# Kernel optimization log

Hardware: AMD Instinct MI355X
Metric: run time of the kernel (lower is better)

The kernel has to match this reference:

```python
import jax, jax.numpy as jnp
import numpy as np

H, DH = 8, 40            # heads, dim_head -> inner_dim = 320
SCALE = DH ** -0.5
B, N, M = 16, 4096, 77   # batch, query tokens (64x64 latent), text tokens
QD, CD, ID = 320, 768, H * DH


def setup_inputs() -> dict:
    key = jax.random.key(0)
    ks = jax.random.split(key, 7)
    x = jax.random.normal(ks[0], (B, N, QD), dtype=jnp.float32)
    context = jax.random.normal(ks[1], (B, M, CD), dtype=jnp.float32)
    # Linear weights stored as (in, out); torch nn.Linear has no bias for q/k/v
    Wq = jax.random.normal(ks[2], (QD, ID), dtype=jnp.float32) * (QD ** -0.5)
    Wk = jax.random.normal(ks[3], (CD, ID), dtype=jnp.float32) * (CD ** -0.5)
    Wv = jax.random.normal(ks[4], (CD, ID), dtype=jnp.float32) * (CD ** -0.5)
    Wo = jax.random.normal(ks[5], (ID, QD), dtype=jnp.float32) * (ID ** -0.5)
    bo = jnp.zeros((QD,), dtype=jnp.float32)
    return {"x": x, "context": context, "Wq": Wq, "Wk": Wk, "Wv": Wv, "Wo": Wo, "bo": bo}


def reference(x, context, Wq, Wk, Wv, Wo, bo):
    b, n, _ = x.shape
    m = context.shape[1]
    q = (x @ Wq).reshape(b, n, H, DH)        # to_q
    k = (context @ Wk).reshape(b, m, H, DH)  # to_k
    v = (context @ Wv).reshape(b, m, H, DH)  # to_v
    # full QK^T * scale (rank-bias path inactive: rank={} / is_add_rank=False)
    scores = jnp.einsum('bihd,bjhd->bhij', q, k) * SCALE  # [B,H,N,M]
    attn = jax.nn.softmax(scores, axis=-1)
    out = jnp.einsum('bhij,bjhd->bihd', attn, v).reshape(b, n, ID)
    return out @ Wo + bo  # to_out Linear; Dropout(p=0.0) is identity
```

## Files before the change

### kernel.cpp

```cpp
#include <hip/hip_runtime.h>

typedef unsigned short u16;
using short8 = __attribute__((ext_vector_type(8))) short;
using f32x4  = __attribute__((ext_vector_type(4))) float;

#define SCALE 0.15811388300841897f

__device__ __forceinline__ u16 f2bf(float f) {
  unsigned int u = __float_as_uint(f);
  u += 0x7fffu + ((u >> 16) & 1u);
  return (u16)(u >> 16);
}


__global__ void prep_transpose(const float* __restrict__ Wq, const float* __restrict__ Wo,
                               const float* __restrict__ Wk, const float* __restrict__ Wv,
                               u16* __restrict__ wqt, u16* __restrict__ wot,
                               u16* __restrict__ wkt, u16* __restrict__ wvt) {
  __shared__ float ld[64][65];
  const int bid = blockIdx.x;
  const float* src; u16* dst; int K; float scale; int tk, tn;
  if (bid < 25)       { src = Wq; dst = wqt; K = 320; scale = SCALE; tk = bid / 5;         tn = bid % 5; }
  else if (bid < 50)  { src = Wo; dst = wot; K = 320; scale = 1.f;   tk = (bid - 25) / 5;  tn = (bid - 25) % 5; }
  else if (bid < 110) { src = Wk; dst = wkt; K = 768; scale = 1.f;   tk = (bid - 50) / 5;  tn = (bid - 50) % 5; }
  else                { src = Wv; dst = wvt; K = 768; scale = 1.f;   tk = (bid - 110) / 5; tn = (bid - 110) % 5; }
  const int c = threadIdx.x & 63, r0 = threadIdx.x >> 6;
  for (int rr = r0; rr < 64; rr += 4)
    ld[rr][c] = src[(size_t)(tk * 64 + rr) * 320 + tn * 64 + c];
  __syncthreads();
  for (int rr = r0; rr < 64; rr += 4)
    dst[(size_t)(tn * 64 + rr) * K + tk * 64 + c] = f2bf(ld[c][rr] * scale);
}

__global__ __launch_bounds__(512, 1)
void kv_mfma(const float* __restrict__ ctx,
             const u16* __restrict__ wkt, const u16* __restrict__ wvt,
             u16* __restrict__ kbf, u16* __restrict__ vt) {
  const int b = blockIdx.x;
  const int tid = threadIdx.x;
  const int w = tid >> 6, l = tid & 63, l16 = l & 15, lhi = l >> 4;
  __shared__ __align__(16) u16 sctx[80][776];

  for (int i = tid; i < 80 * 192; i += 512) {
    int row = i / 192, c4 = (i - row * 192) * 4;
    ushort4 u;
    if (row < 77) {
      float4 v = *reinterpret_cast<const float4*>(&ctx[(size_t)(b * 77 + row) * 768 + c4]);
      u.x = f2bf(v.x); u.y = f2bf(v.y); u.z = f2bf(v.z); u.w = f2bf(v.w);
    } else u = (ushort4){0, 0, 0, 0};
    *reinterpret_cast<ushort4*>(&sctx[row][c4]) = u;
  }
  for (int i = tid; i < 8 * 80 * 3; i += 512) {
    int hm = i / 3, q = i - hm * 3;
    int h = hm / 80, m = hm - h * 80;
    *reinterpret_cast<uint4*>(&kbf[(((size_t)b * 8 + h) * 80 + m) * 64 + 40 + q * 8]) = (uint4){0, 0, 0, 0};
  }
  for (int i = tid; i < 8 * 48 * 2; i += 512) {
    int hd = i / 2, q = i - hd * 2;
    int h = hd / 48, d = hd - h * 48;
    *reinterpret_cast<uint4*>(&vt[(((size_t)b * 8 + h) * 48 + d) * 96 + 80 + q * 8]) = (uint4){0, 0, 0, 0};
  }
  for (int i = tid; i < 8 * 8 * 10; i += 512) {
    int h = i / 80, rem = i - h * 80;
    int d = 40 + rem / 10, q = rem - (rem / 10) * 10;
    *reinterpret_cast<uint4*>(&vt[(((size_t)b * 8 + h) * 48 + d) * 96 + q * 8]) = (uint4){0, 0, 0, 0};
  }
  __syncthreads();

  f32x4 acc[5][5];
  #pragma unroll
  for (int rt = 0; rt < 5; ++rt)
    #pragma unroll
    for (int nt = 0; nt < 5; ++nt) acc[rt][nt] = (f32x4){0.f, 0.f, 0.f, 0.f};

  const u16* wbase = (w < 4) ? (wkt + (size_t)(w * 80) * 768)
                             : (wvt + (size_t)((w - 4) * 80) * 768);
  #pragma unroll 2
  for (int ks = 0; ks < 24; ++ks) {
    short8 af[5];
    #pragma unroll
    for (int rt = 0; rt < 5; ++rt)
      af[rt] = *reinterpret_cast<const short8*>(&sctx[rt * 16 + l16][ks * 32 + lhi * 8]);
    short8 bf[5];
    #pragma unroll
    for (int nt = 0; nt < 5; ++nt)
      bf[nt] = *reinterpret_cast<const short8*>(&wbase[(size_t)(nt * 16 + l16) * 768 + ks * 32 + lhi * 8]);
    #pragma unroll
    for (int rt = 0; rt < 5; ++rt)
      #pragma unroll
      for (int nt = 0; nt < 5; ++nt)
        acc[rt][nt] = __builtin_amdgcn_mfma_f32_16x16x32_bf16(af[rt], bf[nt], acc[rt][nt], 0, 0, 0);
  }

  if (w < 4) {
    #pragma unroll
    for (int rt = 0; rt < 5; ++rt)
      #pragma unroll
      for (int nt = 0; nt < 5; ++nt) {
        int c = w * 80 + nt * 16 + l16, h = c / 40, d = c - h * 40;
        #pragma unroll
        for (int r = 0; r < 4; ++r) {
          int m = rt * 16 + lhi * 4 + r;
          kbf[(((size_t)b * 8 + h) * 80 + m) * 64 + d] = f2bf(m < 77 ? acc[rt][nt][r] : 0.f);
        }
      }
  } else {
    #pragma unroll
    for (int rt = 0; rt < 5; ++rt)
      #pragma unroll
      for (int nt = 0; nt < 5; ++nt) {
        int c = (w - 4) * 80 + nt * 16 + l16, h = c / 40, d = c - h * 40;
        #pragma unroll
        for (int r = 0; r < 4; ++r) {
          int m = rt * 16 + lhi * 4 + r;
          vt[(((size_t)b * 8 + h) * 48 + d) * 96 + m] = f2bf(m < 77 ? acc[rt][nt][r] : 0.f);
        }
      }
  }
}

__global__ __launch_bounds__(256, 3)
void qproj(const float* __restrict__ x, const u16* __restrict__ wqt,
           u16* __restrict__ qg) {
  const int tid = threadIdx.x;
  const int w = tid >> 6, l = tid & 63, l16 = l & 15, lhi = l >> 4;
  const int r0 = blockIdx.x * 64;
  __shared__ __align__(16) u16 xs[64][328];

  const float4* xin = reinterpret_cast<const float4*>(x + (size_t)r0 * 320);
  for (int i = tid; i < 64 * 80; i += 256) {
    float4 v = xin[i];
    int row = i / 80, c4 = (i - row * 80) * 4;
    ushort4 u;
    u.x = f2bf(v.x); u.y = f2bf(v.y); u.z = f2bf(v.z); u.w = f2bf(v.w);
    *reinterpret_cast<ushort4*>(&xs[row][c4]) = u;
  }
  if (blockIdx.x == 1023 && tid < 64) qg[(size_t)65536 * 320 + tid] = 0;
  __syncthreads();

  f32x4 acc[4][5];
  #pragma unroll
  for (int rt = 0; rt < 4; ++rt)
    #pragma unroll
    for (int nt = 0; nt < 5; ++nt) acc[rt][nt] = (f32x4){0.f, 0.f, 0.f, 0.f};
  #pragma unroll 2
  for (int ks = 0; ks < 10; ++ks) {
    short8 af[4];
    #pragma unroll
    for (int rt = 0; rt < 4; ++rt)
      af[rt] = *reinterpret_cast<const short8*>(&xs[rt * 16 + l16][ks * 32 + lhi * 8]);
    #pragma unroll
    for (int nt = 0; nt < 5; ++nt) {
      short8 bf = *reinterpret_cast<const short8*>(&wqt[(size_t)(w * 80 + nt * 16 + l16) * 320 + ks * 32 + lhi * 8]);
      #pragma unroll
      for (int rt = 0; rt < 4; ++rt)
        acc[rt][nt] = __builtin_amdgcn_mfma_f32_16x16x32_bf16(af[rt], bf, acc[rt][nt], 0, 0, 0);
    }
  }
  #pragma unroll
  for (int rt = 0; rt < 4; ++rt)
    #pragma unroll
    for (int nt = 0; nt < 5; ++nt) {
      int col = w * 80 + nt * 16 + l16;
      #pragma unroll
      for (int r = 0; r < 4; ++r) {
        int row = rt * 16 + lhi * 4 + r;
        qg[(size_t)(r0 + row) * 320 + col] = f2bf(acc[rt][nt][r]);
      }
    }
}

__global__ __launch_bounds__(512, 8)
void attn_sm(u16* __restrict__ qg, const u16* __restrict__ kbf,
             const u16* __restrict__ vtp) {
  const int b  = blockIdx.y;
  const int q0 = blockIdx.x * 64;
  const int tid = threadIdx.x;
  const int w   = tid >> 6;
  const int l   = tid & 63;
  const int l16 = l & 15;
  const int lhi = l >> 4;
  const int wq  = w & 3;
  const int hg  = w >> 2;

  __shared__ __align__(16) u16 Pt[8][16][104];

  if (l < 32) {
    int r = l >> 1, q = l & 1;
    *reinterpret_cast<uint4*>(&Pt[w][r][80 + 8 * q]) = (uint4){0u, 0u, 0u, 0u};
  }

  const size_t rowbase = (size_t)(b * 4096 + q0 + wq * 16);

  for (int hi = 0; hi < 4; ++hi) {
    const int h = hg * 4 + hi;
    const u16* kh = kbf + ((size_t)(b * 8 + h)) * 80 * 64;
    const u16* vh = vtp + ((size_t)(b * 8 + h)) * 48 * 96;
    f32x4 sacc[5];
    #pragma unroll
    for (int mt = 0; mt < 5; ++mt) sacc[mt] = (f32x4){0.f, 0.f, 0.f, 0.f};
    #pragma unroll
    for (int ks = 0; ks < 2; ++ks) {
      short8 a = *reinterpret_cast<const short8*>(
          &qg[(rowbase + l16) * 320 + h * 40 + ks * 32 + lhi * 8]);
      #pragma unroll
      for (int mt = 0; mt < 5; ++mt) {
        short8 bb = *reinterpret_cast<const short8*>(&kh[(mt * 16 + l16) * 64 + ks * 32 + lhi * 8]);
        sacc[mt] = __builtin_amdgcn_mfma_f32_16x16x32_bf16(a, bb, sacc[mt], 0, 0, 0);
      }
    }
    #pragma unroll
    for (int r = 0; r < 4; ++r) {
      float sv[5];
      float mx = -1e30f;
      #pragma unroll
      for (int mt = 0; mt < 5; ++mt) {
        float s = sacc[mt][r];
        if (mt * 16 + l16 >= 77) s = -1e30f;
        sv[mt] = s;
        mx = fmaxf(mx, s);
      }
      mx = fmaxf(mx, __shfl_xor(mx, 1));
      mx = fmaxf(mx, __shfl_xor(mx, 2));
      mx = fmaxf(mx, __shfl_xor(mx, 4));
      mx = fmaxf(mx, __shfl_xor(mx, 8));
      float sum = 0.f;
      #pragma unroll
      for (int mt = 0; mt < 5; ++mt) { sv[mt] = __expf(sv[mt] - mx); sum += sv[mt]; }
      sum += __shfl_xor(sum, 1);
      sum += __shfl_xor(sum, 2);
      sum += __shfl_xor(sum, 4);
      sum += __shfl_xor(sum, 8);
      float rs = 1.f / sum;
      int row = lhi * 4 + r;
      #pragma unroll
      for (int mt = 0; mt < 5; ++mt)
        Pt[w][row][mt * 16 + l16] = f2bf(sv[mt] * rs);
    }
    asm volatile("s_waitcnt lgkmcnt(0)" ::: "memory");
    __builtin_amdgcn_sched_barrier(0);
    f32x4 oacc[3];
    #pragma unroll
    for (int nt = 0; nt < 3; ++nt) oacc[nt] = (f32x4){0.f, 0.f, 0.f, 0.f};
    #pragma unroll
    for (int ks = 0; ks < 3; ++ks) {
      short8 a = *reinterpret_cast<const short8*>(&Pt[w][l16][ks * 32 + lhi * 8]);
      #pragma unroll
      for (int nt = 0; nt < 3; ++nt) {
        short8 bb = *reinterpret_cast<const short8*>(&vh[(nt * 16 + l16) * 96 + ks * 32 + lhi * 8]);
        oacc[nt] = __builtin_amdgcn_mfma_f32_16x16x32_bf16(a, bb, oacc[nt], 0, 0, 0);
      }
    }
    asm volatile("s_waitcnt lgkmcnt(0)" ::: "memory");
    __builtin_amdgcn_sched_barrier(0);
    #pragma unroll
    for (int nt = 0; nt < 3; ++nt) {
      int d = nt * 16 + l16;
      if (d < 40) {
        #pragma unroll
        for (int r = 0; r < 4; ++r)
          qg[(rowbase + lhi * 4 + r) * 320 + h * 40 + d] = f2bf(oacc[nt][r]);
      }
    }
  }
}

__global__ __launch_bounds__(256, 4)
void outproj(const u16* __restrict__ og, const u16* __restrict__ wot,
             const float* __restrict__ bo, float* __restrict__ out) {
  const int tid = threadIdx.x;
  const int w = tid >> 6, l = tid & 63, l16 = l & 15, lhi = l >> 4;
  const int r0 = blockIdx.x * 64;
  __shared__ __align__(16) u16 os[64][328];

  for (int i = tid; i < 64 * 40; i += 256) {
    int row = i / 40, c8 = (i - row * 40) * 8;
    *reinterpret_cast<uint4*>(&os[row][c8]) =
        *reinterpret_cast<const uint4*>(&og[(size_t)(r0 + row) * 320 + c8]);
  }
  __syncthreads();

  f32x4 acc[4][5];
  #pragma unroll
  for (int rt = 0; rt < 4; ++rt)
    #pragma unroll
    for (int nt = 0; nt < 5; ++nt) acc[rt][nt] = (f32x4){0.f, 0.f, 0.f, 0.f};
  #pragma unroll 2
  for (int ks = 0; ks < 10; ++ks) {
    short8 af[4];
    #pragma unroll
    for (int rt = 0; rt < 4; ++rt)
      af[rt] = *reinterpret_cast<const short8*>(&os[rt * 16 + l16][ks * 32 + lhi * 8]);
    #pragma unroll
    for (int nt = 0; nt < 5; ++nt) {
      short8 bf = *reinterpret_cast<const short8*>(&wot[(size_t)(w * 80 + nt * 16 + l16) * 320 + ks * 32 + lhi * 8]);
      #pragma unroll
      for (int rt = 0; rt < 4; ++rt)
        acc[rt][nt] = __builtin_amdgcn_mfma_f32_16x16x32_bf16(af[rt], bf, acc[rt][nt], 0, 0, 0);
    }
  }
  #pragma unroll
  for (int nt = 0; nt < 5; ++nt) {
    int col = w * 80 + nt * 16 + l16;
    float bias = bo[col];
    #pragma unroll
    for (int rt = 0; rt < 4; ++rt) {
      #pragma unroll
      for (int r = 0; r < 4; ++r) {
        int row = rt * 16 + lhi * 4 + r;
        out[(size_t)(r0 + row) * 320 + col] = acc[rt][nt][r] + bias;
      }
    }
  }
}

extern "C" void kernel_launch(void* const* d_in, const int* in_sizes, int n_in,
                              void* d_out, int out_size, void* d_ws, size_t ws_size,
                              hipStream_t stream) {
  (void)in_sizes; (void)n_in; (void)out_size; (void)ws_size;
  const float* x       = (const float*)d_in[0];
  const float* context = (const float*)d_in[1];
  const float* Wq      = (const float*)d_in[2];
  const float* Wk      = (const float*)d_in[3];
  const float* Wv      = (const float*)d_in[4];
  const float* Wo      = (const float*)d_in[5];
  const float* bo      = (const float*)d_in[6];
  float* out = (float*)d_out;
  u16* ws = (u16*)d_ws;
  u16* wqt = ws;
  u16* wot = ws + 102400;
  u16* wkt = ws + 204800;
  u16* wvt = ws + 450560;
  u16* kbf = ws + 696320;
  u16* vtp = ws + 1351680;
  u16* qg  = ws + 1941504;

  prep_transpose<<<170, 256, 0, stream>>>(Wq, Wo, Wk, Wv, wqt, wot, wkt, wvt);
  kv_mfma<<<16, 512, 0, stream>>>(context, wkt, wvt, kbf, vtp);
  qproj<<<1024, 256, 0, stream>>>(x, wqt, qg);
  attn_sm<<<dim3(64, 16), 512, 0, stream>>>(qg, kbf, vtp);
  outproj<<<1024, 256, 0, stream>>>(qg, wot, bo, out);
}
```

Baseline: 210.2 us.

## Fuse Q projection into attention kernel and preload weight fragments into registers

New measurement: 372.9 us. +77.4%, slower.

```diff
diff --git a/kernel.cpp b/kernel.cpp
--- a/kernel.cpp
+++ b/kernel.cpp
@@ -119,60 +119,10 @@
   }
 }
 
-__global__ __launch_bounds__(256, 3)
-void qproj(const float* __restrict__ x, const u16* __restrict__ wqt,
-           u16* __restrict__ qg) {
-  const int tid = threadIdx.x;
-  const int w = tid >> 6, l = tid & 63, l16 = l & 15, lhi = l >> 4;
-  const int r0 = blockIdx.x * 64;
-  __shared__ __align__(16) u16 xs[64][328];
-
-  const float4* xin = reinterpret_cast<const float4*>(x + (size_t)r0 * 320);
-  for (int i = tid; i < 64 * 80; i += 256) {
-    float4 v = xin[i];
-    int row = i / 80, c4 = (i - row * 80) * 4;
-    ushort4 u;
-    u.x = f2bf(v.x); u.y = f2bf(v.y); u.z = f2bf(v.z); u.w = f2bf(v.w);
-    *reinterpret_cast<ushort4*>(&xs[row][c4]) = u;
-  }
-  if (blockIdx.x == 1023 && tid < 64) qg[(size_t)65536 * 320 + tid] = 0;
-  __syncthreads();
-
-  f32x4 acc[4][5];
-  #pragma unroll
-  for (int rt = 0; rt < 4; ++rt)
-    #pragma unroll
-    for (int nt = 0; nt < 5; ++nt) acc[rt][nt] = (f32x4){0.f, 0.f, 0.f, 0.f};
-  #pragma unroll 2
-  for (int ks = 0; ks < 10; ++ks) {
-    short8 af[4];
-    #pragma unroll
-    for (int rt = 0; rt < 4; ++rt)
-      af[rt] = *reinterpret_cast<const short8*>(&xs[rt * 16 + l16][ks * 32 + lhi * 8]);
-    #pragma unroll
-    for (int nt = 0; nt < 5; ++nt) {
-      short8 bf = *reinterpret_cast<const short8*>(&wqt[(size_t)(w * 80 + nt * 16 + l16) * 320 + ks * 32 + lhi * 8]);
-      #pragma unroll
-      for (int rt = 0; rt < 4; ++rt)
-        acc[rt][nt] = __builtin_amdgcn_mfma_f32_16x16x32_bf16(af[rt], bf, acc[rt][nt], 0, 0, 0);
-    }
-  }
-  #pragma unroll
-  for (int rt = 0; rt < 4; ++rt)
-    #pragma unroll
-    for (int nt = 0; nt < 5; ++nt) {
-      int col = w * 80 + nt * 16 + l16;
-      #pragma unroll
-      for (int r = 0; r < 4; ++r) {
-        int row = rt * 16 + lhi * 4 + r;
-        qg[(size_t)(r0 + row) * 320 + col] = f2bf(acc[rt][nt][r]);
-      }
-    }
-}
-
-__global__ __launch_bounds__(512, 8)
-void attn_sm(u16* __restrict__ qg, const u16* __restrict__ kbf,
-             const u16* __restrict__ vtp) {
+__global__ __launch_bounds__(512, 4)
+void qattn(const float* __restrict__ x, const u16* __restrict__ wqt,
+           const u16* __restrict__ kbf, const u16* __restrict__ vtp,
+           u16* __restrict__ og) {
   const int b  = blockIdx.y;
   const int q0 = blockIdx.x * 64;
   const int tid = threadIdx.x;
@@ -180,92 +130,150 @@
   const int l   = tid & 63;
   const int l16 = l & 15;
   const int lhi = l >> 4;
-  const int wq  = w & 3;
-  const int hg  = w >> 2;
-
+
+  __shared__ __align__(16) u16 Qx[64][344];
   __shared__ __align__(16) u16 Pt[8][16][104];
 
+  const int ctb = (w < 4) ? 3 * w : 2 * w + 4;
+  int ctv[3];
+  ctv[0] = ctb;
+  ctv[1] = (ctb + 1 < 19) ? ctb + 1 : 19;
+  ctv[2] = (ctb + 2 < 19) ? ctb + 2 : 19;
+
+  short8 wf[10][3];
+  #pragma unroll
+  for (int ks = 0; ks < 10; ++ks)
+    #pragma unroll
+    for (int nt = 0; nt < 3; ++nt)
+      wf[ks][nt] = *reinterpret_cast<const short8*>(
+          &wqt[(size_t)(ctv[nt] * 16 + l16) * 320 + ks * 32 + lhi * 8]);
+
+  const float4* xin = reinterpret_cast<const float4*>(x + (size_t)(b * 4096 + q0) * 320);
+  for (int i = tid; i < 64 * 80; i += 512) {
+    float4 v = xin[i];
+    int row = i / 80, c4 = (i - row * 80) * 4;
+    ushort4 u;
+    u.x = f2bf(v.x); u.y = f2bf(v.y); u.z = f2bf(v.z); u.w = f2bf(v.w);
+    *reinterpret_cast<ushort4*>(&Qx[row][c4]) = u;
+  }
+  for (int i = tid; i < 64 * 6; i += 512) {
+    int row = i / 6, q = i - row * 6;
+    *reinterpret_cast<ushort4*>(&Qx[row][320 + q * 4]) = (ushort4){0, 0, 0, 0};
+  }
   if (l < 32) {
     int r = l >> 1, q = l & 1;
     *reinterpret_cast<uint4*>(&Pt[w][r][80 + 8 * q]) = (uint4){0u, 0u, 0u, 0u};
   }
-
-  const size_t rowbase = (size_t)(b * 4096 + q0 + wq * 16);
-
-  for (int hi = 0; hi < 4; ++hi) {
-    const int h = hg * 4 + hi;
-    const u16* kh = kbf + ((size_t)(b * 8 + h)) * 80 * 64;
-    const u16* vh = vtp + ((size_t)(b * 8 + h)) * 48 * 96;
-    f32x4 sacc[5];
-    #pragma unroll
-    for (int mt = 0; mt < 5; ++mt) sacc[mt] = (f32x4){0.f, 0.f, 0.f, 0.f};
-    #pragma unroll
-    for (int ks = 0; ks < 2; ++ks) {
-      short8 a = *reinterpret_cast<const short8*>(
-          &qg[(rowbase + l16) * 320 + h * 40 + ks * 32 + lhi * 8]);
-      #pragma unroll
-      for (int mt = 0; mt < 5; ++mt) {
-        short8 bb = *reinterpret_cast<const short8*>(&kh[(mt * 16 + l16) * 64 + ks * 32 + lhi * 8]);
-        sacc[mt] = __builtin_amdgcn_mfma_f32_16x16x32_bf16(a, bb, sacc[mt], 0, 0, 0);
-      }
+  __syncthreads();
+
+  {
+    f32x4 qacc[4][3];
+    #pragma unroll
+    for (int rt = 0; rt < 4; ++rt)
+      #pragma unroll
+      for (int nt = 0; nt < 3; ++nt) qacc[rt][nt] = (f32x4){0.f, 0.f, 0.f, 0.f};
+    #pragma unroll 2
+    for (int ks = 0; ks < 10; ++ks) {
+      short8 af[4];
+      #pragma unroll
+      for (int rt = 0; rt < 4; ++rt)
+        af[rt] = *reinterpret_cast<const short8*>(&Qx[rt * 16 + l16][ks * 32 + lhi * 8]);
+      #pragma unroll
+      for (int nt = 0; nt < 3; ++nt)
+        #pragma unroll
+        for (int rt = 0; rt < 4; ++rt)
+          qacc[rt][nt] = __builtin_amdgcn_mfma_f32_16x16x32_bf16(af[rt], wf[ks][nt], qacc[rt][nt], 0, 0, 0);
     }
-    #pragma unroll
-    for (int r = 0; r < 4; ++r) {
-      float sv[5];
-      float mx = -1e30f;
-      #pragma unroll
-      for (int mt = 0; mt < 5; ++mt) {
-        float s = sacc[mt][r];
-        if (mt * 16 + l16 >= 77) s = -1e30f;
-        sv[mt] = s;
-        mx = fmaxf(mx, s);
-      }
-      mx = fmaxf(mx, __shfl_xor(mx, 1));
-      mx = fmaxf(mx, __shfl_xor(mx, 2));
-      mx = fmaxf(mx, __shfl_xor(mx, 4));
-      mx = fmaxf(mx, __shfl_xor(mx, 8));
-      float sum = 0.f;
-      #pragma unroll
-      for (int mt = 0; mt < 5; ++mt) { sv[mt] = __expf(sv[mt] - mx); sum += sv[mt]; }
-      sum += __shfl_xor(sum, 1);
-      sum += __shfl_xor(sum, 2);
-      sum += __shfl_xor(sum, 4);
-      sum += __shfl_xor(sum, 8);
-      float rs = 1.f / sum;
-      int row = lhi * 4 + r;
-      #pragma unroll
-      for (int mt = 0; mt < 5; ++mt)
-        Pt[w][row][mt * 16 + l16] = f2bf(sv[mt] * rs);
+    __syncthreads();
+    #pragma unroll
+    for (int nt = 0; nt < 3; ++nt) {
+      int col = ctv[nt] * 16 + l16;
+      #pragma unroll
+      for (int rt = 0; rt < 4; ++rt)
+        #pragma unroll
+        for (int r = 0; r < 4; ++r)
+          Qx[rt * 16 + lhi * 4 + r][col] = f2bf(qacc[rt][nt][r]);
     }
-    asm volatile("s_waitcnt lgkmcnt(0)" ::: "memory");
-    __builtin_amdgcn_sched_barrier(0);
-    f32x4 oacc[3];
-    #pragma unroll
-    for (int nt = 0; nt < 3; ++nt) oacc[nt] = (f32x4){0.f, 0.f, 0.f, 0.f};
-    #pragma unroll
-    for (int ks = 0; ks < 3; ++ks) {
-      short8 a = *reinterpret_cast<const short8*>(&Pt[w][l16][ks * 32 + lhi * 8]);
+  }
+  __syncthreads();
+
+  {
+    const int wq = w & 3, hg = w >> 2;
+    const size_t orow = (size_t)(b * 4096 + q0 + wq * 16);
+    for (int hi = 0; hi < 4; ++hi) {
+      const int h = hg * 4 + hi;
+      const u16* kh = kbf + (size_t)(b * 8 + h) * 80 * 64;
+      const u16* vh = vtp + (size_t)(b * 8 + h) * 48 * 96;
+      f32x4 sacc[5];
+      #pragma unroll
+      for (int mt = 0; mt < 5; ++mt) sacc[mt] = (f32x4){0.f, 0.f, 0.f, 0.f};
+      #pragma unroll
+      for (int ks = 0; ks < 2; ++ks) {
+        short8 a = *reinterpret_cast<const short8*>(&Qx[wq * 16 + l16][h * 40 + ks * 32 + lhi * 8]);
+        #pragma unroll
+        for (int mt = 0; mt < 5; ++mt) {
+          short8 bb = *reinterpret_cast<const short8*>(&kh[(mt * 16 + l16) * 64 + ks * 32 + lhi * 8]);
+          sacc[mt] = __builtin_amdgcn_mfma_f32_16x16x32_bf16(a, bb, sacc[mt], 0, 0, 0);
+        }
+      }
+      #pragma unroll
+      for (int r = 0; r < 4; ++r) {
+        float sv[5];
+        float mx = -1e30f;
+        #pragma unroll
+        for (int mt = 0; mt < 5; ++mt) {
+          float s = sacc[mt][r];
+          if (mt * 16 + l16 >= 77) s = -1e30f;
+          sv[mt] = s;
+          mx = fmaxf(mx, s);
+        }
+        mx = fmaxf(mx, __shfl_xor(mx, 1));
+        mx = fmaxf(mx, __shfl_xor(mx, 2));
+        mx = fmaxf(mx, __shfl_xor(mx, 4));
+        mx = fmaxf(mx, __shfl_xor(mx, 8));
+        float sum = 0.f;
+        #pragma unroll
+        for (int mt = 0; mt < 5; ++mt) { sv[mt] = __expf(sv[mt] - mx); sum += sv[mt]; }
+        sum += __shfl_xor(sum, 1);
+        sum += __shfl_xor(sum, 2);
+        sum += __shfl_xor(sum, 4);
+        sum += __shfl_xor(sum, 8);
+        float rs = 1.f / sum;
+        int row = lhi * 4 + r;
+        #pragma unroll
+        for (int mt = 0; mt < 5; ++mt)
+          Pt[w][row][mt * 16 + l16] = f2bf(sv[mt] * rs);
+      }
+      asm volatile("s_waitcnt lgkmcnt(0)" ::: "memory");
+      __builtin_amdgcn_sched_barrier(0);
+      f32x4 oacc[3];
+      #pragma unroll
+      for (int nt = 0; nt < 3; ++nt) oacc[nt] = (f32x4){0.f, 0.f, 0.f, 0.f};
+      #pragma unroll
+      for (int ks = 0; ks < 3; ++ks) {
+        short8 a = *reinterpret_cast<const short8*>(&Pt[w][l16][ks * 32 + lhi * 8]);
+        #pragma unroll
+        for (int nt = 0; nt < 3; ++nt) {
+          short8 bb = *reinterpret_cast<const short8*>(&vh[(nt * 16 + l16) * 96 + ks * 32 + lhi * 8]);
+          oacc[nt] = __builtin_amdgcn_mfma_f32_16x16x32_bf16(a, bb, oacc[nt], 0, 0, 0);
+        }
+      }
+      asm volatile("s_waitcnt lgkmcnt(0)" ::: "memory");
+      __builtin_amdgcn_sched_barrier(0);
       #pragma unroll
       for (int nt = 0; nt < 3; ++nt) {
-        short8 bb = *reinterpret_cast<const short8*>(&vh[(nt * 16 + l16) * 96 + ks * 32 + lhi * 8]);
-        oacc[nt] = __builtin_amdgcn_mfma_f32_16x16x32_bf16(a, bb, oacc[nt], 0, 0, 0);
+        int d = nt * 16 + l16;
+        if (d < 40) {
+          #pragma unroll
+          for (int r = 0; r < 4; ++r)
+            og[(orow + lhi * 4 + r) * 320 + h * 40 + d] = f2bf(oacc[nt][r]);
+        }
       }
     }
-    asm volatile("s_waitcnt lgkmcnt(0)" ::: "memory");
-    __builtin_amdgcn_sched_barrier(0);
-    #pragma unroll
-    for (int nt = 0; nt < 3; ++nt) {
-      int d = nt * 16 + l16;
-      if (d < 40) {
-        #pragma unroll
-        for (int r = 0; r < 4; ++r)
-          qg[(rowbase + lhi * 4 + r) * 320 + h * 40 + d] = f2bf(oacc[nt][r]);
-      }
-    }
-  }
-}
-
-__global__ __launch_bounds__(256, 4)
+  }
+}
+
+__global__ __launch_bounds__(256, 3)
 void outproj(const u16* __restrict__ og, const u16* __restrict__ wot,
              const float* __restrict__ bo, float* __restrict__ out) {
   const int tid = threadIdx.x;
@@ -273,6 +281,14 @@
   const int r0 = blockIdx.x * 64;
   __shared__ __align__(16) u16 os[64][328];
 
+  short8 wf[10][5];
+  #pragma unroll
+  for (int ks = 0; ks < 10; ++ks)
+    #pragma unroll
+    for (int nt = 0; nt < 5; ++nt)
+      wf[ks][nt] = *reinterpret_cast<const short8*>(
+          &wot[(size_t)(w * 80 + nt * 16 + l16) * 320 + ks * 32 + lhi * 8]);
+
   for (int i = tid; i < 64 * 40; i += 256) {
     int row = i / 40, c8 = (i - row * 40) * 8;
     *reinterpret_cast<uint4*>(&os[row][c8]) =
@@ -292,12 +308,10 @@
     for (int rt = 0; rt < 4; ++rt)
       af[rt] = *reinterpret_cast<const short8*>(&os[rt * 16 + l16][ks * 32 + lhi * 8]);
     #pragma unroll
-    for (int nt = 0; nt < 5; ++nt) {
-      short8 bf = *reinterpret_cast<const short8*>(&wot[(size_t)(w * 80 + nt * 16 + l16) * 320 + ks * 32 + lhi * 8]);
+    for (int nt = 0; nt < 5; ++nt)
       #pragma unroll
       for (int rt = 0; rt < 4; ++rt)
-        acc[rt][nt] = __builtin_amdgcn_mfma_f32_16x16x32_bf16(af[rt], bf, acc[rt][nt], 0, 0, 0);
-    }
+        acc[rt][nt] = __builtin_amdgcn_mfma_f32_16x16x32_bf16(af[rt], wf[ks][nt], acc[rt][nt], 0, 0, 0);
   }
   #pragma unroll
   for (int nt = 0; nt < 5; ++nt) {
@@ -333,11 +347,10 @@
   u16* wvt = ws + 450560;
   u16* kbf = ws + 696320;
   u16* vtp = ws + 1351680;
-  u16* qg  = ws + 1941504;
+  u16* og  = ws + 1941504;
 
   prep_transpose<<<170, 256, 0, stream>>>(Wq, Wo, Wk, Wv, wqt, wot, wkt, wvt);
   kv_mfma<<<16, 512, 0, stream>>>(context, wkt, wvt, kbf, vtp);
-  qproj<<<1024, 256, 0, stream>>>(x, wqt, qg);
-  attn_sm<<<dim3(64, 16), 512, 0, stream>>>(qg, kbf, vtp);
-  outproj<<<1024, 256, 0, stream>>>(qg, wot, bo, out);
-}
+  qattn<<<dim3(64, 16), 512, 0, stream>>>(x, wqt, kbf, vtp, og);
+  outproj<<<1024, 256, 0, stream>>>(og, wot, bo, out);
+}
```

## Split x bf16 conversion into its own kernel and run Q projection in place

Applied to the files above, without the earlier changes.

After: 225.6 us. +7.3%, slower.

```diff
diff --git a/kernel.cpp b/kernel.cpp
--- a/kernel.cpp
+++ b/kernel.cpp
@@ -32,16 +32,34 @@
     dst[(size_t)(tn * 64 + rr) * K + tk * 64 + c] = f2bf(ld[c][rr] * scale);
 }
 
-__global__ __launch_bounds__(512, 1)
+__global__ __launch_bounds__(256)
+void xconv(const float* __restrict__ x, u16* __restrict__ xbf) {
+  const size_t idx = (size_t)blockIdx.x * 256 + threadIdx.x;
+  const size_t stride = (size_t)gridDim.x * 256;
+  const size_t total = (size_t)65536 * 320 / 8;
+  for (size_t g = idx; g < total; g += stride) {
+    const float4* src = reinterpret_cast<const float4*>(x + g * 8);
+    float4 a = src[0], b = src[1];
+    uint4 o;
+    o.x = (unsigned)f2bf(a.x) | ((unsigned)f2bf(a.y) << 16);
+    o.y = (unsigned)f2bf(a.z) | ((unsigned)f2bf(a.w) << 16);
+    o.z = (unsigned)f2bf(b.x) | ((unsigned)f2bf(b.y) << 16);
+    o.w = (unsigned)f2bf(b.z) | ((unsigned)f2bf(b.w) << 16);
+    *reinterpret_cast<uint4*>(xbf + g * 8) = o;
+  }
+  if (blockIdx.x == 0 && threadIdx.x < 64) xbf[(size_t)65536 * 320 + threadIdx.x] = 0;
+}
+
+__global__ __launch_bounds__(256, 1)
 void kv_mfma(const float* __restrict__ ctx,
              const u16* __restrict__ wkt, const u16* __restrict__ wvt,
              u16* __restrict__ kbf, u16* __restrict__ vt) {
-  const int b = blockIdx.x;
+  const int b = blockIdx.x, z = blockIdx.y;
   const int tid = threadIdx.x;
   const int w = tid >> 6, l = tid & 63, l16 = l & 15, lhi = l >> 4;
   __shared__ __align__(16) u16 sctx[80][776];
 
-  for (int i = tid; i < 80 * 192; i += 512) {
+  for (int i = tid; i < 80 * 192; i += 256) {
     int row = i / 192, c4 = (i - row * 192) * 4;
     ushort4 u;
     if (row < 77) {
@@ -50,20 +68,23 @@
     } else u = (ushort4){0, 0, 0, 0};
     *reinterpret_cast<ushort4*>(&sctx[row][c4]) = u;
   }
-  for (int i = tid; i < 8 * 80 * 3; i += 512) {
-    int hm = i / 3, q = i - hm * 3;
-    int h = hm / 80, m = hm - h * 80;
-    *reinterpret_cast<uint4*>(&kbf[(((size_t)b * 8 + h) * 80 + m) * 64 + 40 + q * 8]) = (uint4){0, 0, 0, 0};
-  }
-  for (int i = tid; i < 8 * 48 * 2; i += 512) {
-    int hd = i / 2, q = i - hd * 2;
-    int h = hd / 48, d = hd - h * 48;
-    *reinterpret_cast<uint4*>(&vt[(((size_t)b * 8 + h) * 48 + d) * 96 + 80 + q * 8]) = (uint4){0, 0, 0, 0};
-  }
-  for (int i = tid; i < 8 * 8 * 10; i += 512) {
-    int h = i / 80, rem = i - h * 80;
-    int d = 40 + rem / 10, q = rem - (rem / 10) * 10;
-    *reinterpret_cast<uint4*>(&vt[(((size_t)b * 8 + h) * 48 + d) * 96 + q * 8]) = (uint4){0, 0, 0, 0};
+  if (z == 0) {
+    for (int i = tid; i < 8 * 80 * 3; i += 256) {
+      int hm = i / 3, q = i - hm * 3;
+      int h = hm / 80, m = hm - h * 80;
+      *reinterpret_cast<uint4*>(&kbf[(((size_t)b * 8 + h) * 80 + m) * 64 + 40 + q * 8]) = (uint4){0, 0, 0, 0};
+    }
+  } else {
+    for (int i = tid; i < 8 * 48 * 2; i += 256) {
+      int hd = i / 2, q = i - hd * 2;
+      int h = hd / 48, d = hd - h * 48;
+      *reinterpret_cast<uint4*>(&vt[(((size_t)b * 8 + h) * 48 + d) * 96 + 80 + q * 8]) = (uint4){0, 0, 0, 0};
+    }
+    for (int i = tid; i < 8 * 8 * 10; i += 256) {
+      int h = i / 80, rem = i - h * 80;
+      int d = 40 + rem / 10, q = rem - (rem / 10) * 10;
+      *reinterpret_cast<uint4*>(&vt[(((size_t)b * 8 + h) * 48 + d) * 96 + q * 8]) = (uint4){0, 0, 0, 0};
+    }
   }
   __syncthreads();
 
@@ -73,8 +94,7 @@
     #pragma unroll
     for (int nt = 0; nt < 5; ++nt) acc[rt][nt] = (f32x4){0.f, 0.f, 0.f, 0.f};
 
-  const u16* wbase = (w < 4) ? (wkt + (size_t)(w * 80) * 768)
-                             : (wvt + (size_t)((w - 4) * 80) * 768);
+  const u16* wbase = (z == 0 ? wkt : wvt) + (size_t)(w * 80) * 768;
   #pragma unroll 2
   for (int ks = 0; ks < 24; ++ks) {
     short8 af[5];
@@ -92,7 +112,7 @@
         acc[rt][nt] = __builtin_amdgcn_mfma_f32_16x16x32_bf16(af[rt], bf[nt], acc[rt][nt], 0, 0, 0);
   }
 
-  if (w < 4) {
+  if (z == 0) {
     #pragma unroll
     for (int rt = 0; rt < 5; ++rt)
       #pragma unroll
@@ -109,7 +129,7 @@
     for (int rt = 0; rt < 5; ++rt)
       #pragma unroll
       for (int nt = 0; nt < 5; ++nt) {
-        int c = (w - 4) * 80 + nt * 16 + l16, h = c / 40, d = c - h * 40;
+        int c = w * 80 + nt * 16 + l16, h = c / 40, d = c - h * 40;
         #pragma unroll
         for (int r = 0; r < 4; ++r) {
           int m = rt * 16 + lhi * 4 + r;
@@ -120,22 +140,17 @@
 }
 
 __global__ __launch_bounds__(256, 3)
-void qproj(const float* __restrict__ x, const u16* __restrict__ wqt,
-           u16* __restrict__ qg) {
+void qproj(u16* __restrict__ qg, const u16* __restrict__ wqt) {
   const int tid = threadIdx.x;
   const int w = tid >> 6, l = tid & 63, l16 = l & 15, lhi = l >> 4;
   const int r0 = blockIdx.x * 64;
   __shared__ __align__(16) u16 xs[64][328];
 
-  const float4* xin = reinterpret_cast<const float4*>(x + (size_t)r0 * 320);
-  for (int i = tid; i < 64 * 80; i += 256) {
-    float4 v = xin[i];
-    int row = i / 80, c4 = (i - row * 80) * 4;
-    ushort4 u;
-    u.x = f2bf(v.x); u.y = f2bf(v.y); u.z = f2bf(v.z); u.w = f2bf(v.w);
-    *reinterpret_cast<ushort4*>(&xs[row][c4]) = u;
-  }
-  if (blockIdx.x == 1023 && tid < 64) qg[(size_t)65536 * 320 + tid] = 0;
+  for (int i = tid; i < 64 * 40; i += 256) {
+    int row = i / 40, c8 = (i - row * 40) * 8;
+    *reinterpret_cast<uint4*>(&xs[row][c8]) =
+        *reinterpret_cast<const uint4*>(&qg[(size_t)(r0 + row) * 320 + c8]);
+  }
   __syncthreads();
 
   f32x4 acc[4][5];
@@ -157,17 +172,22 @@
         acc[rt][nt] = __builtin_amdgcn_mfma_f32_16x16x32_bf16(af[rt], bf, acc[rt][nt], 0, 0, 0);
     }
   }
+  __syncthreads();
   #pragma unroll
   for (int rt = 0; rt < 4; ++rt)
     #pragma unroll
     for (int nt = 0; nt < 5; ++nt) {
       int col = w * 80 + nt * 16 + l16;
       #pragma unroll
-      for (int r = 0; r < 4; ++r) {
-        int row = rt * 16 + lhi * 4 + r;
-        qg[(size_t)(r0 + row) * 320 + col] = f2bf(acc[rt][nt][r]);
-      }
-    }
+      for (int r = 0; r < 4; ++r)
+        xs[rt * 16 + lhi * 4 + r][col] = f2bf(acc[rt][nt][r]);
+    }
+  __syncthreads();
+  for (int i = tid; i < 64 * 40; i += 256) {
+    int row = i / 40, c8 = (i - row * 40) * 8;
+    *reinterpret_cast<uint4*>(&qg[(size_t)(r0 + row) * 320 + c8]) =
+        *reinterpret_cast<const uint4*>(&xs[row][c8]);
+  }
 }
 
 __global__ __launch_bounds__(512, 8)
@@ -336,8 +356,9 @@
   u16* qg  = ws + 1941504;
 
   prep_transpose<<<170, 256, 0, stream>>>(Wq, Wo, Wk, Wv, wqt, wot, wkt, wvt);
-  kv_mfma<<<16, 512, 0, stream>>>(context, wkt, wvt, kbf, vtp);
-  qproj<<<1024, 256, 0, stream>>>(x, wqt, qg);
+  xconv<<<2048, 256, 0, stream>>>(x, qg);
+  kv_mfma<<<dim3(16, 2), 256, 0, stream>>>(context, wkt, wvt, kbf, vtp);
+  qproj<<<1024, 256, 0, stream>>>(qg, wqt);
   attn_sm<<<dim3(64, 16), 512, 0, stream>>>(qg, kbf, vtp);
   outproj<<<1024, 256, 0, stream>>>(qg, wot, bo, out);
 }
```
